# Kernel tuning notes

Hardware: AMD Instinct MI355X
Metric: run time of the kernel (lower is better)

The kernel has to match this reference:

```python
import jax, jax.numpy as jnp
import numpy as np

N_NODES = 50000
N_EDGES = 800000
D_FEAT = 128
DIM_H = 128
N_LAYERS = 3
N_CLASSES = 10
N_GRAPHS = 512


def setup_inputs() -> dict:
    key = jax.random.key(0)
    ks = jax.random.split(key, 8)
    x = jax.random.normal(ks[0], (N_NODES, D_FEAT), dtype=jnp.float32)
    W = jax.random.normal(ks[1], (N_LAYERS, DIM_H, DIM_H), dtype=jnp.float32) * 0.1
    b = jnp.zeros((N_LAYERS, DIM_H), dtype=jnp.float32)
    lin_w = jax.random.normal(ks[2], (DIM_H, N_CLASSES), dtype=jnp.float32) * 0.1
    lin_b = jnp.zeros((N_CLASSES,), dtype=jnp.float32)
    edge_index = jax.random.randint(ks[3], (2, N_EDGES), 0, N_NODES, dtype=jnp.int64)
    batch = jnp.sort(jax.random.randint(ks[4], (N_NODES,), 0, N_GRAPHS, dtype=jnp.int64))
    return {"x": x, "W": W, "b": b, "lin_w": lin_w, "lin_b": lin_b,
            "edge_index": edge_index, "batch": batch, "num_layers": N_LAYERS}


def _gcn_norm(edge_index, n_nodes):
    # add self loops (PyG GCNConv default), then symmetric normalization
    loop = jnp.arange(n_nodes, dtype=edge_index.dtype)
    src = jnp.concatenate([edge_index[0], loop])  # [E+N]
    dst = jnp.concatenate([edge_index[1], loop])
    deg = jax.ops.segment_sum(jnp.ones_like(dst, dtype=jnp.float32), dst,
                              num_segments=n_nodes)
    dinv = jnp.where(deg > 0, jax.lax.rsqrt(deg), 0.0)
    norm = dinv[src] * dinv[dst]  # [E+N]
    return src, dst, norm


def _gcn_conv(h, Wi, bi, src, dst, norm, n_nodes):
    h = h @ Wi                       # [N, dim_h] dense GEMM
    msg = h[src] * norm[:, None]     # gather + scale, [E+N, dim_h]
    out = jax.ops.segment_sum(msg, dst, num_segments=n_nodes)  # scatter-add
    return out + bi


def reference(x, W, b, lin_w, lin_b, edge_index, batch, num_layers):
    n_nodes = x.shape[0]
    src, dst, norm = _gcn_norm(edge_index, n_nodes)
    h = x
    for i in range(num_layers):
        h = jax.nn.relu(_gcn_conv(h, W[i], b[i], src, dst, norm, n_nodes))
    # global mean pool over graph ids
    sums = jax.ops.segment_sum(h, batch, num_segments=N_GRAPHS)          # [G, dim_h]
    cnts = jax.ops.segment_sum(jnp.ones((n_nodes,), h.dtype), batch,
                               num_segments=N_GRAPHS)
    hG = sums / jnp.maximum(cnts, 1.0)[:, None]
    # dropout is identity at eval; num_layers > 1 branch applies the linear head
    logits = hG @ lin_w + lin_b
    return hG, jax.nn.log_softmax(logits, axis=1)
```

## Files before the change

### kernel.cpp

```cpp
#include <hip/hip_runtime.h>
#include <hip/hip_bf16.h>
#include <hip/hip_fp8.h>

#define NN 50000
#define NE 800000
#define FD 128
#define NG 512
#define NC 10
#define NL 3
#define CAP 64
#define GEMM_B 782
#define CVT_B 128
#define COMP_B 910
#define CHUNKS 782
#define NXCD 8
#define NODES_PER_XCD 6250
#define FRONT_B 8190
#define PATCH_B 12500

typedef unsigned short u16;
typedef unsigned char u8;
typedef unsigned int u32;
typedef short bf16x8 __attribute__((ext_vector_type(8)));
typedef float f32x4 __attribute__((ext_vector_type(4)));
typedef float f32x2 __attribute__((ext_vector_type(2)));

__device__ __forceinline__ float b2f(u16 v) {
    union { u32 u; float f; } c; c.u = ((u32)v) << 16; return c.f;
}
__device__ __forceinline__ u16 f2b(float f) {
    __hip_bfloat16 h = __float2bfloat16(f);
    return *(u16*)&h;
}
__device__ __forceinline__ float p2f(u8 b) {
    __hip_fp8_e4m3 h; h.__x = b; return (float)h;
}
__device__ __forceinline__ u8 f2p(float f) {
    __hip_fp8_e4m3 h(f); return h.__x;
}

#if defined(__has_builtin)
#if __has_builtin(__builtin_amdgcn_cvt_pk_f32_fp8)
#define HAVE_PKCVT 1
#endif
#endif
template<bool HI>
__device__ __forceinline__ f32x2 pkcvt(u32 u) {
#ifdef HAVE_PKCVT
    return __builtin_amdgcn_cvt_pk_f32_fp8((int)u, HI);
#else
    f32x2 r;
    r[0] = p2f((u8)(HI ? (u >> 16) : u));
    r[1] = p2f((u8)(HI ? (u >> 24) : (u >> 8)));
    return r;
#endif
}

__global__ __launch_bounds__(256) void k_front(const int* __restrict__ src,
                                               const int* __restrict__ dst,
                                               int* __restrict__ cnt,
                                               int* __restrict__ bkt,
                                               const float* __restrict__ W,
                                               u16* __restrict__ wt,
                                               const float* __restrict__ x,
                                               u8* __restrict__ Bout) {
    const int bid = blockIdx.x;
    if (bid % 9 == 0) {
        const int q = bid / 9;
        if (q < GEMM_B) {
            const int wid = q * 4 + (threadIdx.x >> 6);
            if (wid >= 3125) return;
            const int row0 = wid * 16;
            const int lane = threadIdx.x & 63;
            const int m = lane & 15;
            const int qq = lane >> 4;
            f32x4 acc[8];
#pragma unroll
            for (int ct = 0; ct < 8; ++ct) acc[ct] = (f32x4){0.f, 0.f, 0.f, 0.f};
            const float* arow = x + (size_t)(row0 + m) * FD + qq * 8;
            const float* wbase = W + (size_t)qq * 8 * FD + m;
#pragma unroll
            for (int kb = 0; kb < 4; ++kb) {
                const float4 p0 = *(const float4*)(arow + kb * 32);
                const float4 p1 = *(const float4*)(arow + kb * 32 + 4);
                bf16x8 af;
                af[0] = (short)f2b(p0.x); af[1] = (short)f2b(p0.y);
                af[2] = (short)f2b(p0.z); af[3] = (short)f2b(p0.w);
                af[4] = (short)f2b(p1.x); af[5] = (short)f2b(p1.y);
                af[6] = (short)f2b(p1.z); af[7] = (short)f2b(p1.w);
#pragma unroll
                for (int ct = 0; ct < 8; ++ct) {
                    const float* wp = wbase + (size_t)kb * 32 * FD + ct * 16;
                    bf16x8 bf;
#pragma unroll
                    for (int j = 0; j < 8; ++j)
                        bf[j] = (short)f2b(wp[(size_t)j * FD]);
                    acc[ct] = __builtin_amdgcn_mfma_f32_16x16x32_bf16(af, bf,
                                                                      acc[ct], 0, 0, 0);
                }
            }
#pragma unroll
            for (int ct = 0; ct < 8; ++ct)
#pragma unroll
                for (int r = 0; r < 4; ++r)
                    Bout[(size_t)(row0 + qq * 4 + r) * FD + ct * 16 + m] =
                        f2p(acc[ct][r]);
        } else {
            const int c = (q - GEMM_B) * 256 + threadIdx.x + FD * FD;
            const int l = c >> 14, rr = c & 16383, k = rr >> 7, n = rr & 127;
            wt[(l << 14) + n * FD + k] = f2b(W[c]);
        }
        return;
    }
    const int bin = bid & 7;
    const int t = bid >> 3;
    const int m0 = 9 * bin;
    const int c9 = (bid > m0) ? ((bid - m0 - 1) / 72 + 1) : 0;
    const int chunk = t - c9;
    if (chunk >= CHUNKS) return;
    const int e0 = chunk * 1024 + (threadIdx.x << 2);
    if (e0 >= NE) return;
    const int4 d4 = *(const int4*)(dst + e0);
    const int dd[4] = {d4.x, d4.y, d4.z, d4.w};
#pragma unroll
    for (int j = 0; j < 4; ++j) {
        const int d = dd[j];
        if ((u32)d / (u32)NODES_PER_XCD == (u32)bin) {
            const int s = src[e0 + j];
            const int slot = atomicAdd(&cnt[d], 1);
            if (slot < CAP) bkt[d * CAP + slot] = s;
        }
    }
}

__global__ __launch_bounds__(256) void k_patch(const int* __restrict__ cnt,
                                               int* __restrict__ bkt) {
    const int i = blockIdx.x * 256 + threadIdx.x;
    const int d = i >> 6;
    const int s = i & 63;
    if (s < cnt[d]) {
        const int v = bkt[i];
        const u32 w = (u32)f2b(rsqrtf((float)(cnt[v] + 1)));
        bkt[i] = (int)(((u32)v & 0xFFFFu) | (w << 16));
    }
}

template<bool W8>
__device__ __forceinline__ float4 gather_node(const int rs, const int re,
                                              const int* __restrict__ bkt,
                                              const u8* __restrict__ B,
                                              const float di, const int n,
                                              const float4 bb, const int f) {
    const u32 us = *(const u32*)(B + (size_t)n * FD + f);
    f32x2 aL0 = {0.f, 0.f}, aL1 = {0.f, 0.f}, aL2 = {0.f, 0.f}, aL3 = {0.f, 0.f};
    f32x2 aH0 = {0.f, 0.f}, aH1 = {0.f, 0.f}, aH2 = {0.f, 0.f}, aH3 = {0.f, 0.f};
    int e = rs;
    if (W8) {
        for (; e + 8 <= re; e += 8) {
            const int4 p0 = *(const int4*)(bkt + e);
            const int4 p1 = *(const int4*)(bkt + e + 4);
            const u32 r0 = *(const u32*)(B + (size_t)(p0.x & 0xFFFF) * FD + f);
            const u32 r1 = *(const u32*)(B + (size_t)(p0.y & 0xFFFF) * FD + f);
            const u32 r2 = *(const u32*)(B + (size_t)(p0.z & 0xFFFF) * FD + f);
            const u32 r3 = *(const u32*)(B + (size_t)(p0.w & 0xFFFF) * FD + f);
            const u32 r4 = *(const u32*)(B + (size_t)(p1.x & 0xFFFF) * FD + f);
            const u32 r5 = *(const u32*)(B + (size_t)(p1.y & 0xFFFF) * FD + f);
            const u32 r6 = *(const u32*)(B + (size_t)(p1.z & 0xFFFF) * FD + f);
            const u32 r7 = *(const u32*)(B + (size_t)(p1.w & 0xFFFF) * FD + f);
            const float w0 = b2f((u16)((u32)p0.x >> 16));
            const float w1 = b2f((u16)((u32)p0.y >> 16));
            const float w2 = b2f((u16)((u32)p0.z >> 16));
            const float w3 = b2f((u16)((u32)p0.w >> 16));
            const float w4 = b2f((u16)((u32)p1.x >> 16));
            const float w5 = b2f((u16)((u32)p1.y >> 16));
            const float w6 = b2f((u16)((u32)p1.z >> 16));
            const float w7 = b2f((u16)((u32)p1.w >> 16));
            aL0 += pkcvt<false>(r0) * w0; aH0 += pkcvt<true>(r0) * w0;
            aL1 += pkcvt<false>(r1) * w1; aH1 += pkcvt<true>(r1) * w1;
            aL2 += pkcvt<false>(r2) * w2; aH2 += pkcvt<true>(r2) * w2;
            aL3 += pkcvt<false>(r3) * w3; aH3 += pkcvt<true>(r3) * w3;
            aL0 += pkcvt<false>(r4) * w4; aH0 += pkcvt<true>(r4) * w4;
            aL1 += pkcvt<false>(r5) * w5; aH1 += pkcvt<true>(r5) * w5;
            aL2 += pkcvt<false>(r6) * w6; aH2 += pkcvt<true>(r6) * w6;
            aL3 += pkcvt<false>(r7) * w7; aH3 += pkcvt<true>(r7) * w7;
        }
    }
    for (; e + 4 <= re; e += 4) {
        const int4 p0 = *(const int4*)(bkt + e);
        const u32 r0 = *(const u32*)(B + (size_t)(p0.x & 0xFFFF) * FD + f);
        const u32 r1 = *(const u32*)(B + (size_t)(p0.y & 0xFFFF) * FD + f);
        const u32 r2 = *(const u32*)(B + (size_t)(p0.z & 0xFFFF) * FD + f);
        const u32 r3 = *(const u32*)(B + (size_t)(p0.w & 0xFFFF) * FD + f);
        const float w0 = b2f((u16)((u32)p0.x >> 16));
        const float w1 = b2f((u16)((u32)p0.y >> 16));
        const float w2 = b2f((u16)((u32)p0.z >> 16));
        const float w3 = b2f((u16)((u32)p0.w >> 16));
        aL0 += pkcvt<false>(r0) * w0; aH0 += pkcvt<true>(r0) * w0;
        aL1 += pkcvt<false>(r1) * w1; aH1 += pkcvt<true>(r1) * w1;
        aL2 += pkcvt<false>(r2) * w2; aH2 += pkcvt<true>(r2) * w2;
        aL3 += pkcvt<false>(r3) * w3; aH3 += pkcvt<true>(r3) * w3;
    }
    for (; e < re; ++e) {
        const int pk = bkt[e];
        const u32 r0 = *(const u32*)(B + (size_t)(pk & 0xFFFF) * FD + f);
        const float w0 = b2f((u16)((u32)pk >> 16));
        aL0 += pkcvt<false>(r0) * w0; aH0 += pkcvt<true>(r0) * w0;
    }
    aL0 += pkcvt<false>(us) * di;
    aH0 += pkcvt<true>(us) * di;
    const f32x2 L = (aL0 + aL1) + (aL2 + aL3);
    const f32x2 H = (aH0 + aH1) + (aH2 + aH3);
    float4 r;
    r.x = fmaxf(fmaf(L[0], di, bb.x), 0.f);
    r.y = fmaxf(fmaf(L[1], di, bb.y), 0.f);
    r.z = fmaxf(fmaf(H[0], di, bb.z), 0.f);
    r.w = fmaxf(fmaf(H[1], di, bb.w), 0.f);
    return r;
}

__global__ __launch_bounds__(512) void k_gg(const int* __restrict__ cnt,
                                            const int* __restrict__ bkt,
                                            const u8* __restrict__ Bin,
                                            const float* __restrict__ bias,
                                            const u16* __restrict__ WTn,
                                            u8* __restrict__ Bout) {
    __shared__ u16 sA[16][FD + 8];
    const int tid = threadIdx.x;
    const int wave = tid >> 6;
    const int lane = tid & 63;
    const int nb = blockIdx.x * 16;
    {
        const int half = lane >> 5;
        const int n = nb + wave * 2 + half;
        const int f = (lane & 31) * 4;
        const int cn = cnt[n];
        const int rs = n * CAP;
        const float di = rsqrtf((float)(cn + 1));
        const float4 bb = *(const float4*)(bias + f);
        const float4 r = gather_node<true>(rs, rs + cn, bkt, Bin, di, n, bb, f);
        ushort4 o;
        o.x = f2b(r.x); o.y = f2b(r.y); o.z = f2b(r.z); o.w = f2b(r.w);
        *(ushort4*)&sA[wave * 2 + half][f] = o;
    }
    __syncthreads();
    const int ct = wave;
    const int m = lane & 15;
    const int q = lane >> 4;
    f32x4 acc = (f32x4){0.f, 0.f, 0.f, 0.f};
    const u16* wrow = WTn + (size_t)m * FD + q * 8 + (size_t)ct * 16 * FD;
#pragma unroll
    for (int kb = 0; kb < 4; ++kb) {
        bf16x8 af = *(const bf16x8*)&sA[m][q * 8 + kb * 32];
        bf16x8 bf = *(const bf16x8*)(wrow + kb * 32);
        acc = __builtin_amdgcn_mfma_f32_16x16x32_bf16(af, bf, acc, 0, 0, 0);
    }
#pragma unroll
    for (int r = 0; r < 4; ++r)
        Bout[(size_t)(nb + q * 4 + r) * FD + ct * 16 + m] = f2p(acc[r]);
}

__global__ __launch_bounds__(1024) void k_gpool(const int* __restrict__ cnt,
                                                const int* __restrict__ bkt,
                                                const u8* __restrict__ B,
                                                const float* __restrict__ bias,
                                                const int* __restrict__ batch,
                                                const float* __restrict__ lin_w,
                                                const float* __restrict__ lin_b,
                                                float* __restrict__ out) {
    __shared__ float sfeat[32][FD + 4];
    __shared__ float hm[FD];
    __shared__ int bnd[2];
    __shared__ float part2[2 * NC];
    const int g = blockIdx.x;
    const int tid = threadIdx.x;
    const int lane = tid & 63;
    const int slot = (tid >> 6) * 2 + (lane >> 5);
    const int f = (lane & 31) * 4;
    if (tid < 2) {
        const int key = g + tid;
        int lo = 0, hi = NN;
        while (lo < hi) {
            const int mid = (lo + hi) >> 1;
            if (batch[mid] < key) lo = mid + 1; else hi = mid;
        }
        bnd[tid] = lo;
    }
    __syncthreads();
    const int r0 = bnd[0], r1 = bnd[1];
    const float4 bb = *(const float4*)(bias + f);
    float s0 = 0.f, s1 = 0.f, s2 = 0.f, s3 = 0.f;
    for (int r = r0 + slot; r < r1; r += 32) {
        const int cn = cnt[r];
        const int rs = r * CAP;
        const float di = rsqrtf((float)(cn + 1));
        const float4 v = gather_node<false>(rs, rs + cn, bkt, B, di, r, bb, f);
        s0 += v.x; s1 += v.y; s2 += v.z; s3 += v.w;
    }
    sfeat[slot][f] = s0;
    sfeat[slot][f + 1] = s1;
    sfeat[slot][f + 2] = s2;
    sfeat[slot][f + 3] = s3;
    __syncthreads();
    if (tid < 128) {
        float tot = 0.f;
#pragma unroll
        for (int s = 0; s < 32; ++s) tot += sfeat[s][tid];
        const float mean = tot / fmaxf((float)(r1 - r0), 1.0f);
        hm[tid] = mean;
        out[(size_t)g * FD + tid] = mean;
    }
    __syncthreads();
    if (tid < 128) {
        const float hv = hm[tid];
        const int wv = tid >> 6;
#pragma unroll
        for (int c = 0; c < NC; ++c) {
            float p = hv * lin_w[tid * NC + c];
#pragma unroll
            for (int o = 32; o > 0; o >>= 1) p += __shfl_down(p, o, 64);
            if ((tid & 63) == 0) part2[c * 2 + wv] = p;
        }
    }
    __syncthreads();
    if (tid == 0) {
        float lg[NC];
        float m = -1e30f;
#pragma unroll
        for (int c = 0; c < NC; ++c) {
            lg[c] = part2[2 * c] + part2[2 * c + 1] + lin_b[c];
            m = fmaxf(m, lg[c]);
        }
        float s = 0.f;
#pragma unroll
        for (int c = 0; c < NC; ++c) s += expf(lg[c] - m);
        const float lse = m + logf(s);
        float* o = out + (size_t)NG * FD + (size_t)g * NC;
#pragma unroll
        for (int c = 0; c < NC; ++c) o[c] = lg[c] - lse;
    }
}

extern "C" void kernel_launch(void* const* d_in, const int* in_sizes, int n_in,
                              void* d_out, int out_size, void* d_ws, size_t ws_size,
                              hipStream_t stream) {
    const float* x     = (const float*)d_in[0];
    const float* W     = (const float*)d_in[1];
    const float* bias  = (const float*)d_in[2];
    const float* lin_w = (const float*)d_in[3];
    const float* lin_b = (const float*)d_in[4];
    const int*   src   = (const int*)d_in[5];
    const int*   dst   = src + NE;
    const int*   batch = (const int*)d_in[6];

    u8*    B0     = (u8*)d_ws;
    u8*    B1     = B0 + (size_t)NN * FD;
    u16*   WT     = (u16*)(B1 + (size_t)NN * FD);
    int*   bkt    = (int*)(WT + (size_t)NL * FD * FD);
    int*   cnt    = bkt + (size_t)NN * CAP;
    float* out    = (float*)d_out;

    (void)hipMemsetAsync(cnt, 0, NN * sizeof(int), stream);
    k_front<<<FRONT_B, 256, 0, stream>>>(src, dst, cnt, bkt, W, WT, x, B0);
    k_patch<<<PATCH_B, 256, 0, stream>>>(cnt, bkt);

    k_gg<<<NN / 16, 512, 0, stream>>>(cnt, bkt, B0, bias,
                                      WT + (size_t)1 * FD * FD, B1);
    k_gg<<<NN / 16, 512, 0, stream>>>(cnt, bkt, B1, bias + FD,
                                      WT + (size_t)2 * FD * FD, B0);
    k_gpool<<<NG, 1024, 0, stream>>>(cnt, bkt, B0, bias + 2 * FD,
                                     batch, lin_w, lin_b, out);
}
```

Before: 228.7 us.

## Build CSR buckets via two-pass binned partition instead of global atomics

Replaces the XCD-binned global-atomic bucket fill with a two-phase partition. Edges are first histogrammed into 256-node bins in shared memory and scattered to per-bin buffers reusing the B1 workspace. A per-bin block then builds the 64-slot adjacency lists in LDS and writes them out coalesced. This removes 800k global atomics on per-node counters and the 9x redundant dst scanning, at the cost of an extra kernel launch, an intermediate buffer pass, and a fixed per-bin capacity (BCAP) that could drop edges if exceeded.

```diff
diff --git a/kernel.cpp b/kernel.cpp
--- a/kernel.cpp
+++ b/kernel.cpp
@@ -10,12 +10,12 @@
 #define NL 3
 #define CAP 64
 #define GEMM_B 782
-#define CVT_B 128
 #define COMP_B 910
-#define CHUNKS 782
-#define NXCD 8
-#define NODES_PER_XCD 6250
-#define FRONT_B 8190
+#define NBIN 196
+#define BCAP 4800
+#define CHUNK 4096
+#define NCHUNK 196
+#define PART_B (NCHUNK + COMP_B)
 #define PATCH_B 12500
 
 typedef unsigned short u16;
@@ -56,22 +56,28 @@
 #endif
 }
 
-__global__ __launch_bounds__(256) void k_front(const int* __restrict__ src,
-                                               const int* __restrict__ dst,
-                                               int* __restrict__ cnt,
-                                               int* __restrict__ bkt,
-                                               const float* __restrict__ W,
-                                               u16* __restrict__ wt,
-                                               const float* __restrict__ x,
-                                               u8* __restrict__ Bout) {
+__global__ __launch_bounds__(256) void k_part(const int* __restrict__ src,
+                                              const int* __restrict__ dst,
+                                              int* __restrict__ gcnt,
+                                              int* __restrict__ ebuf,
+                                              const float* __restrict__ W,
+                                              u16* __restrict__ wt,
+                                              const float* __restrict__ x,
+                                              u8* __restrict__ Bout) {
+    __shared__ int stage[CHUNK];
+    __shared__ int hist[NBIN];
+    __shared__ int lbase[NBIN];
+    __shared__ int gbase[NBIN];
+    __shared__ int scan[256];
     const int bid = blockIdx.x;
-    if (bid % 9 == 0) {
-        const int q = bid / 9;
+    const int tid = threadIdx.x;
+    if (bid >= NCHUNK) {
+        const int q = bid - NCHUNK;
         if (q < GEMM_B) {
-            const int wid = q * 4 + (threadIdx.x >> 6);
+            const int wid = q * 4 + (tid >> 6);
             if (wid >= 3125) return;
             const int row0 = wid * 16;
-            const int lane = threadIdx.x & 63;
+            const int lane = tid & 63;
             const int m = lane & 15;
             const int qq = lane >> 4;
             f32x4 acc[8];
@@ -106,31 +112,86 @@
                     Bout[(size_t)(row0 + qq * 4 + r) * FD + ct * 16 + m] =
                         f2p(acc[ct][r]);
         } else {
-            const int c = (q - GEMM_B) * 256 + threadIdx.x + FD * FD;
+            const int c = (q - GEMM_B) * 256 + tid + FD * FD;
             const int l = c >> 14, rr = c & 16383, k = rr >> 7, n = rr & 127;
             wt[(l << 14) + n * FD + k] = f2b(W[c]);
         }
         return;
     }
-    const int bin = bid & 7;
-    const int t = bid >> 3;
-    const int m0 = 9 * bin;
-    const int c9 = (bid > m0) ? ((bid - m0 - 1) / 72 + 1) : 0;
-    const int chunk = t - c9;
-    if (chunk >= CHUNKS) return;
-    const int e0 = chunk * 1024 + (threadIdx.x << 2);
-    if (e0 >= NE) return;
-    const int4 d4 = *(const int4*)(dst + e0);
-    const int dd[4] = {d4.x, d4.y, d4.z, d4.w};
-#pragma unroll
-    for (int j = 0; j < 4; ++j) {
-        const int d = dd[j];
-        if ((u32)d / (u32)NODES_PER_XCD == (u32)bin) {
-            const int s = src[e0 + j];
-            const int slot = atomicAdd(&cnt[d], 1);
-            if (slot < CAP) bkt[d * CAP + slot] = s;
-        }
-    }
+    if (tid < NBIN) hist[tid] = 0;
+    __syncthreads();
+    const int e00 = bid * CHUNK;
+    int dv[16], sv[16], pp[16];
+#pragma unroll
+    for (int k = 0; k < 4; ++k) {
+        const int e = e00 + k * 1024 + tid * 4;
+        if (e < NE) {
+            const int4 d4 = *(const int4*)(dst + e);
+            const int4 s4 = *(const int4*)(src + e);
+            dv[k*4+0] = d4.x; dv[k*4+1] = d4.y; dv[k*4+2] = d4.z; dv[k*4+3] = d4.w;
+            sv[k*4+0] = s4.x; sv[k*4+1] = s4.y; sv[k*4+2] = s4.z; sv[k*4+3] = s4.w;
+        } else {
+            dv[k*4+0] = dv[k*4+1] = dv[k*4+2] = dv[k*4+3] = -1;
+        }
+    }
+#pragma unroll
+    for (int k = 0; k < 16; ++k)
+        if (dv[k] >= 0) pp[k] = atomicAdd(&hist[((u32)dv[k]) >> 8], 1);
+    __syncthreads();
+    const int hv = (tid < NBIN) ? hist[tid] : 0;
+    scan[tid] = hv;
+    __syncthreads();
+    for (int o = 1; o < 256; o <<= 1) {
+        const int t = (tid >= o) ? scan[tid - o] : 0;
+        __syncthreads();
+        scan[tid] += t;
+        __syncthreads();
+    }
+    if (tid < NBIN) {
+        lbase[tid] = scan[tid] - hv;
+        gbase[tid] = atomicAdd(&gcnt[tid], hv);
+    }
+    const int total = scan[255];
+    __syncthreads();
+#pragma unroll
+    for (int k = 0; k < 16; ++k)
+        if (dv[k] >= 0)
+            stage[lbase[((u32)dv[k]) >> 8] + pp[k]] = (dv[k] << 16) | sv[k];
+    __syncthreads();
+    for (int i = tid; i < total; i += 256) {
+        const int pv = stage[i];
+        const int b = ((u32)pv) >> 24;
+        const int idx = gbase[b] + (i - lbase[b]);
+        if (idx < BCAP) ebuf[(size_t)b * BCAP + idx] = pv;
+    }
+}
+
+__global__ __launch_bounds__(256) void k_build(const int* __restrict__ gcnt,
+                                               const int* __restrict__ ebuf,
+                                               int* __restrict__ cnt,
+                                               int* __restrict__ bkt) {
+    __shared__ int cl[256];
+    __shared__ int bl[256 * CAP];
+    const int b = blockIdx.x;
+    const int tid = threadIdx.x;
+    cl[tid] = 0;
+    __syncthreads();
+    const int m = min(gcnt[b], BCAP);
+    const int* eb = ebuf + (size_t)b * BCAP;
+    for (int i = tid; i < m; i += 256) {
+        const int pv = eb[i];
+        const int ld = (((u32)pv) >> 16) & 255;
+        const int slot = atomicAdd(&cl[ld], 1);
+        if (slot < CAP) bl[ld * CAP + slot] = pv & 0xFFFF;
+    }
+    __syncthreads();
+    const int n0 = b * 256;
+    const int nh = min(256, NN - n0);
+    if (tid < nh) cnt[n0 + tid] = cl[tid];
+    int4* dstp = (int4*)(bkt + (size_t)n0 * CAP);
+    const int4* srcp = (const int4*)bl;
+    const int ti = nh * (CAP / 4);
+    for (int i = tid; i < ti; i += 256) dstp[i] = srcp[i];
 }
 
 __global__ __launch_bounds__(256) void k_patch(const int* __restrict__ cnt,
@@ -357,10 +418,13 @@
     u16*   WT     = (u16*)(B1 + (size_t)NN * FD);
     int*   bkt    = (int*)(WT + (size_t)NL * FD * FD);
     int*   cnt    = bkt + (size_t)NN * CAP;
+    int*   gcnt   = cnt + NN;
+    int*   ebuf   = (int*)B1;
     float* out    = (float*)d_out;
 
-    (void)hipMemsetAsync(cnt, 0, NN * sizeof(int), stream);
-    k_front<<<FRONT_B, 256, 0, stream>>>(src, dst, cnt, bkt, W, WT, x, B0);
+    (void)hipMemsetAsync(gcnt, 0, NBIN * sizeof(int), stream);
+    k_part<<<PART_B, 256, 0, stream>>>(src, dst, gcnt, ebuf, W, WT, x, B0);
+    k_build<<<NBIN, 256, 0, stream>>>(gcnt, ebuf, cnt, bkt);
     k_patch<<<PATCH_B, 256, 0, stream>>>(cnt, bkt);
 
     k_gg<<<NN / 16, 512, 0, stream>>>(cnt, bkt, B0, bias,
```

New measurement: 213.3 us. 6.7% less time.
